# Kernel tuning notes

Measured on AMD Instinct MI355X. Metric: run time of the kernel, lower is better.

The kernel has to match this reference:

```python
import jax, jax.numpy as jnp
import numpy as np

D_MODEL = 1024
N_HEADS = 16
D_HEAD = D_MODEL // N_HEADS
LSR_RANK = 32
B, T = 2, 2048


def setup_inputs() -> dict:
    key = jax.random.key(0)
    ks = jax.random.split(key, 12)
    s = 1.0 / np.sqrt(D_MODEL)
    return {
        "x": jax.random.normal(ks[0], (B, T, D_MODEL), dtype=jnp.float32),
        "Wq": jax.random.normal(ks[1], (D_MODEL, D_MODEL), dtype=jnp.float32) * s,
        "bq": jnp.zeros((D_MODEL,), dtype=jnp.float32),
        "Wk": jax.random.normal(ks[2], (D_MODEL, D_MODEL), dtype=jnp.float32) * s,
        "bk": jnp.zeros((D_MODEL,), dtype=jnp.float32),
        "Wv": jax.random.normal(ks[3], (D_MODEL, D_MODEL), dtype=jnp.float32) * s,
        "bv": jnp.zeros((D_MODEL,), dtype=jnp.float32),
        "Wo": jax.random.normal(ks[4], (D_MODEL, D_MODEL), dtype=jnp.float32) * s,
        "bo": jnp.zeros((D_MODEL,), dtype=jnp.float32),
        "Wq_lsr": jax.random.normal(ks[5], (N_HEADS, D_HEAD, LSR_RANK), dtype=jnp.float32),
        "Wk_lsr": jax.random.normal(ks[6], (N_HEADS, D_HEAD, LSR_RANK), dtype=jnp.float32),
    }


def reference(x, Wq, bq, Wk, bk, Wv, bv, Wo, bo, Wq_lsr, Wk_lsr):
    Bn, Tn, dm = x.shape
    H, Dh, R = Wq_lsr.shape
    # q/k/v projections, split into heads: (B, H, T, Dh)
    def split_heads(y):
        return y.reshape(Bn, Tn, H, Dh).transpose(0, 2, 1, 3)
    q = split_heads(x @ Wq + bq)
    k = split_heads(x @ Wk + bk)
    v = split_heads(x @ Wv + bv)
    # low-rank projected scores: (Q Wq_lsr)(K Wk_lsr)^T / sqrt(R)
    q_lr = jnp.einsum('bhtd,hdr->bhtr', q, Wq_lsr)
    k_lr = jnp.einsum('bhtd,hdr->bhtr', k, Wk_lsr)
    scale = 1.0 / jnp.sqrt(jnp.float32(R))
    scores = jnp.einsum('bhir,bhjr->bhij', q_lr, k_lr) * scale
    # causal mask
    causal = jnp.tril(jnp.ones((Tn, Tn), dtype=bool))
    scores = jnp.where(causal[None, None], scores, -jnp.inf)
    attn = jax.nn.softmax(scores, axis=-1)
    out = jnp.einsum('bhij,bhjd->bhid', attn, v)  # (B, H, T, Dh)
    out = out.transpose(0, 2, 1, 3).reshape(Bn, Tn, dm)
    return out @ Wo + bo
```

## Files before the change

kernel.cpp:

```cpp
#include <hip/hip_runtime.h>
#include <math.h>

#define D_MODEL 1024
#define N_HEADS 16
#define D_HEAD  64
#define LSR_RANK 32
#define BATCH 2
#define SEQ 2048
#define M_TOT (BATCH*SEQ)

typedef __attribute__((ext_vector_type(8))) short short8v;
typedef __attribute__((ext_vector_type(4))) short short4v;
typedef __attribute__((ext_vector_type(4))) float f32x4;

static __device__ __forceinline__ ushort bfhi(float f) {
    union { float f; unsigned u; } c; c.f = f;
    return (ushort)(c.u >> 16);
}
static __device__ __forceinline__ float bff(ushort h) {
    union { unsigned u; float f; } c; c.u = ((unsigned)h) << 16;
    return c.f;
}
static __device__ __forceinline__ ushort f2bf_rn(float f) {
    union { float f; unsigned u; } c; c.f = f;
    unsigned r = c.u + 0x7FFF + ((c.u >> 16) & 1);
    return (ushort)(r >> 16);
}
static __device__ __forceinline__ void split8(const float4 a, const float4 b,
                                              short8v& h, short8v& l) {
    ushort h0 = bfhi(a.x), h1 = bfhi(a.y), h2 = bfhi(a.z), h3 = bfhi(a.w);
    ushort h4 = bfhi(b.x), h5 = bfhi(b.y), h6 = bfhi(b.z), h7 = bfhi(b.w);
    h[0] = (short)h0; h[1] = (short)h1; h[2] = (short)h2; h[3] = (short)h3;
    h[4] = (short)h4; h[5] = (short)h5; h[6] = (short)h6; h[7] = (short)h7;
    l[0] = (short)bfhi(a.x - bff(h0)); l[1] = (short)bfhi(a.y - bff(h1));
    l[2] = (short)bfhi(a.z - bff(h2)); l[3] = (short)bfhi(a.w - bff(h3));
    l[4] = (short)bfhi(b.x - bff(h4)); l[5] = (short)bfhi(b.y - bff(h5));
    l[6] = (short)bfhi(b.z - bff(h6)); l[7] = (short)bfhi(b.w - bff(h7));
}
static __device__ __forceinline__ void trunc8(const float4 a, const float4 b,
                                              short8v& h) {
    h[0] = (short)bfhi(a.x); h[1] = (short)bfhi(a.y);
    h[2] = (short)bfhi(a.z); h[3] = (short)bfhi(a.w);
    h[4] = (short)bfhi(b.x); h[5] = (short)bfhi(b.y);
    h[6] = (short)bfhi(b.z); h[7] = (short)bfhi(b.w);
}

__global__ __launch_bounds__(256) void eff_weight2(
    const float* __restrict__ Wq, const float* __restrict__ Wq_lsr,
    const float* __restrict__ Wk, const float* __restrict__ Wk_lsr,
    float* __restrict__ Weff_tmp)
{
    const int z = blockIdx.y;
    const float* W    = z ? Wk : Wq;
    const float* Wlsr = z ? Wk_lsr : Wq_lsr;
    const int base = z << 9;
    int idx = blockIdx.x * 256 + threadIdx.x;
    int k = idx >> 9;
    int c = idx & 511;
    int h = c >> 5;
    int r = c & 31;
    const float* wrow = W + (size_t)k * D_MODEL + h * D_HEAD;
    const float* lsr  = Wlsr + (size_t)h * D_HEAD * LSR_RANK + r;
    float acc = 0.f;
    #pragma unroll
    for (int d = 0; d < D_HEAD; ++d)
        acc = fmaf(wrow[d], lsr[d * LSR_RANK], acc);
    Weff_tmp[(size_t)k * 1024 + base + c] = acc;
}

__global__ __launch_bounds__(256) void eff_bias_kernel(
    const float* __restrict__ bq, const float* __restrict__ Wq_lsr,
    const float* __restrict__ bk, const float* __restrict__ Wk_lsr,
    const float* __restrict__ bv, float* __restrict__ bcat)
{
    int c = blockIdx.x * 256 + threadIdx.x;
    if (c < 1024) {
        const float* bias = (c < 512) ? bq : bk;
        const float* lsr  = (c < 512) ? Wq_lsr : Wk_lsr;
        int cc = c & 511;
        int h = cc >> 5, r = cc & 31;
        float acc = 0.f;
        #pragma unroll
        for (int d = 0; d < D_HEAD; ++d)
            acc = fmaf(bias[h * D_HEAD + d],
                       lsr[(size_t)h * D_HEAD * LSR_RANK + d * LSR_RANK + r], acc);
        bcat[c] = acc;
    } else {
        bcat[c] = bv[c - 1024];
    }
}

__global__ __launch_bounds__(256) void transpose2(
    const float* __restrict__ in0, float* __restrict__ out0,
    const float* __restrict__ in1, float* __restrict__ out1)
{
    const float* in  = blockIdx.z ? in1 : in0;
    float* out       = blockIdx.z ? out1 : out0;
    __shared__ float t[64][65];
    const int tid = threadIdx.x;
    const int r0 = blockIdx.y * 64, c0 = blockIdx.x * 64;
    const int tr = tid >> 4, tc = tid & 15;
    #pragma unroll
    for (int i = 0; i < 4; ++i) {
        float4 v = *(const float4*)&in[(size_t)(r0 + tr + i * 16) * 1024 + c0 + tc * 4];
        t[tr + i * 16][tc * 4 + 0] = v.x;
        t[tr + i * 16][tc * 4 + 1] = v.y;
        t[tr + i * 16][tc * 4 + 2] = v.z;
        t[tr + i * 16][tc * 4 + 3] = v.w;
    }
    __syncthreads();
    #pragma unroll
    for (int i = 0; i < 4; ++i) {
        float4 v;
        v.x = t[tc * 4 + 0][tr + i * 16];
        v.y = t[tc * 4 + 1][tr + i * 16];
        v.z = t[tc * 4 + 2][tr + i * 16];
        v.w = t[tc * 4 + 3][tr + i * 16];
        *(float4*)&out[(size_t)(c0 + tr + i * 16) * 1024 + r0 + tc * 4] = v;
    }
}

__global__ __launch_bounds__(256) void tsplit_rn1024(
    const float* __restrict__ in, ushort* __restrict__ out)
{
    __shared__ float t[64][65];
    const int tid = threadIdx.x;
    const int r0 = blockIdx.y * 64, c0 = blockIdx.x * 64;
    const int tr = tid >> 4, tc = tid & 15;
    #pragma unroll
    for (int i = 0; i < 4; ++i) {
        float4 v = *(const float4*)&in[(size_t)(r0 + tr + i * 16) * 1024 + c0 + tc * 4];
        t[tr + i * 16][tc * 4 + 0] = v.x;
        t[tr + i * 16][tc * 4 + 1] = v.y;
        t[tr + i * 16][tc * 4 + 2] = v.z;
        t[tr + i * 16][tc * 4 + 3] = v.w;
    }
    __syncthreads();
    #pragma unroll
    for (int i = 0; i < 4; ++i) {
        short4v hv = {(short)f2bf_rn(t[tc * 4 + 0][tr + i * 16]),
                      (short)f2bf_rn(t[tc * 4 + 1][tr + i * 16]),
                      (short)f2bf_rn(t[tc * 4 + 2][tr + i * 16]),
                      (short)f2bf_rn(t[tc * 4 + 3][tr + i * 16])};
        *(short4v*)&out[(size_t)(c0 + tr + i * 16) * 1024 + r0 + tc * 4] = hv;
    }
}

__global__ __launch_bounds__(256) void gemm_proj_fused(
    const float* __restrict__ x,
    const float* __restrict__ Wcat_t,
    const float* __restrict__ bcat,
    float* __restrict__ Yqk,
    short* __restrict__ Kth, short* __restrict__ Ktl,
    short* __restrict__ Vbf)
{
    __shared__ __align__(16) short Ah[128 * 40], Al[128 * 40];
    __shared__ __align__(16) short Bh[128 * 40], Bl[128 * 40];

    const int tid = threadIdx.x;
    const int bx = blockIdx.x;
    const int m0 = blockIdx.y * 128, n0 = bx * 128;
    const bool vhalf = (bx >= 8);
    const int wid = tid >> 6, wr = wid >> 1, wc = wid & 1;
    const int lane = tid & 63, fr = lane & 15, fq = lane >> 4;
    const int srow = tid >> 1;
    const int skq  = (tid & 1) << 4;

    f32x4 acc[4][4];
    #pragma unroll
    for (int i = 0; i < 4; ++i)
        #pragma unroll
        for (int j = 0; j < 4; ++j)
            acc[i][j] = (f32x4){0.f, 0.f, 0.f, 0.f};

    const float* Ag = x + (size_t)(m0 + srow) * 1024 + skq;
    const float* Bg = Wcat_t + (size_t)(n0 + srow) * 1024 + skq;
    short* pAh = &Ah[srow * 40 + skq];
    short* pAl = &Al[srow * 40 + skq];
    short* pBh = &Bh[srow * 40 + skq];
    short* pBl = &Bl[srow * 40 + skq];

    for (int k0 = 0; k0 < 1024; k0 += 32) {
        float4 a0 = *(const float4*)(Ag + k0);
        float4 a1 = *(const float4*)(Ag + k0 + 4);
        float4 a2 = *(const float4*)(Ag + k0 + 8);
        float4 a3 = *(const float4*)(Ag + k0 + 12);
        float4 b0 = *(const float4*)(Bg + k0);
        float4 b1 = *(const float4*)(Bg + k0 + 4);
        float4 b2 = *(const float4*)(Bg + k0 + 8);
        float4 b3 = *(const float4*)(Bg + k0 + 12);
        if (vhalf) {
            short8v h;
            trunc8(a0, a1, h); *(short8v*)pAh = h;
            trunc8(a2, a3, h); *(short8v*)(pAh + 8) = h;
            trunc8(b0, b1, h); *(short8v*)pBh = h;
            trunc8(b2, b3, h); *(short8v*)(pBh + 8) = h;
        } else {
            short8v h, l;
            split8(a0, a1, h, l);
            *(short8v*)pAh = h;  *(short8v*)pAl = l;
            split8(a2, a3, h, l);
            *(short8v*)(pAh + 8) = h;  *(short8v*)(pAl + 8) = l;
            split8(b0, b1, h, l);
            *(short8v*)pBh = h;  *(short8v*)pBl = l;
            split8(b2, b3, h, l);
            *(short8v*)(pBh + 8) = h;  *(short8v*)(pBl + 8) = l;
        }
        __syncthreads();

        short8v afh[4], bfh[4];
        #pragma unroll
        for (int fi = 0; fi < 4; ++fi)
            afh[fi] = *(const short8v*)&Ah[(wr * 64 + fi * 16 + fr) * 40 + fq * 8];
        #pragma unroll
        for (int bj = 0; bj < 4; ++bj)
            bfh[bj] = *(const short8v*)&Bh[(wc * 64 + bj * 16 + fr) * 40 + fq * 8];

        if (vhalf) {
            #pragma unroll
            for (int fi = 0; fi < 4; ++fi)
                #pragma unroll
                for (int bj = 0; bj < 4; ++bj)
                    acc[fi][bj] = __builtin_amdgcn_mfma_f32_16x16x32_bf16(
                        afh[fi], bfh[bj], acc[fi][bj], 0, 0, 0);
        } else {
            short8v afl[4], bfl[4];
            #pragma unroll
            for (int fi = 0; fi < 4; ++fi)
                afl[fi] = *(const short8v*)&Al[(wr * 64 + fi * 16 + fr) * 40 + fq * 8];
            #pragma unroll
            for (int bj = 0; bj < 4; ++bj)
                bfl[bj] = *(const short8v*)&Bl[(wc * 64 + bj * 16 + fr) * 40 + fq * 8];
            #pragma unroll
            for (int fi = 0; fi < 4; ++fi) {
                #pragma unroll
                for (int bj = 0; bj < 4; ++bj) {
                    acc[fi][bj] = __builtin_amdgcn_mfma_f32_16x16x32_bf16(
                        afh[fi], bfh[bj], acc[fi][bj], 0, 0, 0);
                    acc[fi][bj] = __builtin_amdgcn_mfma_f32_16x16x32_bf16(
                        afh[fi], bfl[bj], acc[fi][bj], 0, 0, 0);
                    acc[fi][bj] = __builtin_amdgcn_mfma_f32_16x16x32_bf16(
                        afl[fi], bfh[bj], acc[fi][bj], 0, 0, 0);
                }
            }
        }
        __syncthreads();
    }

    const int b = m0 >> 11;
    #pragma unroll
    for (int fi = 0; fi < 4; ++fi) {
        #pragma unroll
        for (int bj = 0; bj < 4; ++bj) {
            const int r = m0 + wr * 64 + fi * 16 + fq * 4;
            const int gcol = n0 + wc * 64 + bj * 16 + fr;
            const float bv_ = bcat[gcol];
            if (bx < 4) {
                #pragma unroll
                for (int j = 0; j < 4; ++j)
                    Yqk[(size_t)(r + j) * 1024 + gcol] = acc[fi][bj][j] + bv_;
            } else if (bx < 8) {
                const int kc = gcol - 512;
                const int h = kc >> 5, rr = kc & 31;
                short* oh = Kth + (((size_t)(b * 16 + h) * 2048) + (r & 2047)) * 32 + rr;
                short* ol = Ktl + (((size_t)(b * 16 + h) * 2048) + (r & 2047)) * 32 + rr;
                #pragma unroll
                for (int j = 0; j < 4; ++j) {
                    const float v = acc[fi][bj][j] + bv_;
                    const ushort vh = bfhi(v);
                    oh[j * 32] = (short)vh;
                    ol[j * 32] = (short)bfhi(v - bff(vh));
                }
            } else {
                const int vc = gcol - 1024;
                const int h = vc >> 6, d = vc & 63;
                short4v o = {(short)f2bf_rn(acc[fi][bj][0] + bv_),
                             (short)f2bf_rn(acc[fi][bj][1] + bv_),
                             (short)f2bf_rn(acc[fi][bj][2] + bv_),
                             (short)f2bf_rn(acc[fi][bj][3] + bv_)};
                *(short4v*)&Vbf[((size_t)(b * 16 + h) * 64 + d) * 2048 + (r & 2047)] = o;
            }
        }
    }
}

__global__ __launch_bounds__(256) void gemm_out_bf(
    const ushort* __restrict__ Obf,
    const ushort* __restrict__ Wot,
    const float* __restrict__ bo,
    float* __restrict__ out)
{
    __shared__ __align__(16) short Ah[128 * 40];
    __shared__ __align__(16) short Bh[128 * 40];

    const int tid = threadIdx.x;
    const int m0 = blockIdx.y * 128, n0 = blockIdx.x * 128;
    const int wid = tid >> 6, wr = wid >> 1, wc = wid & 1;
    const int lane = tid & 63, fr = lane & 15, fq = lane >> 4;
    const int srow = tid >> 1;
    const int skq  = (tid & 1) << 4;

    f32x4 acc[4][4];
    #pragma unroll
    for (int i = 0; i < 4; ++i)
        #pragma unroll
        for (int j = 0; j < 4; ++j)
            acc[i][j] = (f32x4){0.f, 0.f, 0.f, 0.f};

    const ushort* AgH = Obf + (size_t)(m0 + srow) * 1024 + skq;
    const ushort* BgH = Wot + (size_t)(n0 + srow) * 1024 + skq;
    short* pAh = &Ah[srow * 40 + skq];
    short* pBh = &Bh[srow * 40 + skq];

    for (int k0 = 0; k0 < 1024; k0 += 32) {
        *(short8v*)pAh       = *(const short8v*)(AgH + k0);
        *(short8v*)(pAh + 8) = *(const short8v*)(AgH + k0 + 8);
        *(short8v*)pBh       = *(const short8v*)(BgH + k0);
        *(short8v*)(pBh + 8) = *(const short8v*)(BgH + k0 + 8);
        __syncthreads();

        short8v afh[4], bfh[4];
        #pragma unroll
        for (int fi = 0; fi < 4; ++fi)
            afh[fi] = *(const short8v*)&Ah[(wr * 64 + fi * 16 + fr) * 40 + fq * 8];
        #pragma unroll
        for (int bj = 0; bj < 4; ++bj)
            bfh[bj] = *(const short8v*)&Bh[(wc * 64 + bj * 16 + fr) * 40 + fq * 8];
        #pragma unroll
        for (int fi = 0; fi < 4; ++fi)
            #pragma unroll
            for (int bj = 0; bj < 4; ++bj)
                acc[fi][bj] = __builtin_amdgcn_mfma_f32_16x16x32_bf16(
                    afh[fi], bfh[bj], acc[fi][bj], 0, 0, 0);
        __syncthreads();
    }

    #pragma unroll
    for (int fi = 0; fi < 4; ++fi) {
        #pragma unroll
        for (int bj = 0; bj < 4; ++bj) {
            const int r = m0 + wr * 64 + fi * 16 + fq * 4;
            const int c = n0 + wc * 64 + bj * 16 + fr;
            const float bv_ = bo[c];
            #pragma unroll
            for (int j = 0; j < 4; ++j)
                out[(size_t)(r + j) * 1024 + c] = acc[fi][bj][j] + bv_;
        }
    }
}

#define P_LD  68
#define MASKVAL (-1e30f)

__global__ __launch_bounds__(512) void flash_mfma(
    const float* __restrict__ Yqk,
    const short* __restrict__ Kth, const short* __restrict__ Ktl,
    const short* __restrict__ Vbf,
    ushort* __restrict__ Obf)
{
    const float scale = 0.1767766952966369f;
    const int L = blockIdx.x;
    const int bh = L & 31;
    const int qt = 31 - (L >> 5);
    const int b = bh >> 4, h = bh & 15;
    const int tid = threadIdx.x;
    const int w = tid >> 6;
    const int g = w & 3;
    const int p = w >> 2;
    const int lane = tid & 63;
    const int fr = lane & 15, fq = lane >> 4;

    __shared__ __align__(16) short Pall[8][16 * P_LD];
    __shared__ __align__(16) char exraw[4 * 64 * 80];
    short* Pw = &Pall[w][0];

    short8v aqh, aql;
    {
        const float* qp = Yqk + (size_t)(b * SEQ + qt * 64 + g * 16 + fr) * 1024
                          + h * 32 + fq * 8;
        split8(*(const float4*)qp, *(const float4*)(qp + 4), aqh, aql);
    }

    f32x4 acc0 = {0,0,0,0}, acc1 = {0,0,0,0}, acc2 = {0,0,0,0}, acc3 = {0,0,0,0};
    float m_[4], l_[4];
    #pragma unroll
    for (int r = 0; r < 4; ++r) { m_[r] = MASKVAL; l_[r] = 0.f; }

    const short* kb_h = Kth + (size_t)bh * 2048 * 32;
    const short* kb_l = Ktl + (size_t)bh * 2048 * 32;
    const short* vb   = Vbf + (size_t)bh * 64 * 2048;
    const int kidx = fr * 32 + fq * 8;
    const int vrow = fr * 2048 + fq * 8;

    for (int jt = p; jt <= qt; jt += 2) {
        const short* kp_h = kb_h + (size_t)jt * 64 * 32;
        const short* kp_l = kb_l + (size_t)jt * 64 * 32;
        short8v kh0 = *(const short8v*)&kp_h[kidx];
        short8v kh1 = *(const short8v*)&kp_h[kidx + 512];
        short8v kh2 = *(const short8v*)&kp_h[kidx + 1024];
        short8v kh3 = *(const short8v*)&kp_h[kidx + 1536];
        short8v kl0 = *(const short8v*)&kp_l[kidx];
        short8v kl1 = *(const short8v*)&kp_l[kidx + 512];
        short8v kl2 = *(const short8v*)&kp_l[kidx + 1024];
        short8v kl3 = *(const short8v*)&kp_l[kidx + 1536];
        const short* vp = vb + vrow + jt * 64;
        short8v v00 = *(const short8v*)&vp[0];
        short8v v01 = *(const short8v*)&vp[32];
        short8v v10 = *(const short8v*)&vp[16 * 2048];
        short8v v11 = *(const short8v*)&vp[16 * 2048 + 32];
        short8v v20 = *(const short8v*)&vp[32 * 2048];
        short8v v21 = *(const short8v*)&vp[32 * 2048 + 32];
        short8v v30 = *(const short8v*)&vp[48 * 2048];
        short8v v31 = *(const short8v*)&vp[48 * 2048 + 32];

        f32x4 s0 = {0,0,0,0}, s1 = {0,0,0,0}, s2 = {0,0,0,0}, s3 = {0,0,0,0};
        s0 = __builtin_amdgcn_mfma_f32_16x16x32_bf16(aqh, kh0, s0, 0, 0, 0);
        s0 = __builtin_amdgcn_mfma_f32_16x16x32_bf16(aqh, kl0, s0, 0, 0, 0);
        s0 = __builtin_amdgcn_mfma_f32_16x16x32_bf16(aql, kh0, s0, 0, 0, 0);
        s1 = __builtin_amdgcn_mfma_f32_16x16x32_bf16(aqh, kh1, s1, 0, 0, 0);
        s1 = __builtin_amdgcn_mfma_f32_16x16x32_bf16(aqh, kl1, s1, 0, 0, 0);
        s1 = __builtin_amdgcn_mfma_f32_16x16x32_bf16(aql, kh1, s1, 0, 0, 0);
        s2 = __builtin_amdgcn_mfma_f32_16x16x32_bf16(aqh, kh2, s2, 0, 0, 0);
        s2 = __builtin_amdgcn_mfma_f32_16x16x32_bf16(aqh, kl2, s2, 0, 0, 0);
        s2 = __builtin_amdgcn_mfma_f32_16x16x32_bf16(aql, kh2, s2, 0, 0, 0);
        s3 = __builtin_amdgcn_mfma_f32_16x16x32_bf16(aqh, kh3, s3, 0, 0, 0);
        s3 = __builtin_amdgcn_mfma_f32_16x16x32_bf16(aqh, kl3, s3, 0, 0, 0);
        s3 = __builtin_amdgcn_mfma_f32_16x16x32_bf16(aql, kh3, s3, 0, 0, 0);

        s0 *= scale; s1 *= scale; s2 *= scale; s3 *= scale;

        if (jt == qt) {
            #pragma unroll
            for (int r = 0; r < 4; ++r) {
                const int q_l = g * 16 + fq * 4 + r;
                s0[r] = (fr      <= q_l) ? s0[r] : MASKVAL;
                s1[r] = (16 + fr <= q_l) ? s1[r] : MASKVAL;
                s2[r] = (32 + fr <= q_l) ? s2[r] : MASKVAL;
                s3[r] = (48 + fr <= q_l) ? s3[r] : MASKVAL;
            }
        }

        float al[4];
        #pragma unroll
        for (int r = 0; r < 4; ++r) {
            float mt = fmaxf(fmaxf(s0[r], s1[r]), fmaxf(s2[r], s3[r]));
            mt = fmaxf(mt, __shfl_xor(mt, 1));
            mt = fmaxf(mt, __shfl_xor(mt, 2));
            mt = fmaxf(mt, __shfl_xor(mt, 4));
            mt = fmaxf(mt, __shfl_xor(mt, 8));
            const float mnew = fmaxf(m_[r], mt);
            al[r] = __expf(m_[r] - mnew);
            m_[r] = mnew;
            s0[r] = __expf(s0[r] - mnew);
            s1[r] = __expf(s1[r] - mnew);
            s2[r] = __expf(s2[r] - mnew);
            s3[r] = __expf(s3[r] - mnew);
            float ps = s0[r] + s1[r] + s2[r] + s3[r];
            ps += __shfl_xor(ps, 1);
            ps += __shfl_xor(ps, 2);
            ps += __shfl_xor(ps, 4);
            ps += __shfl_xor(ps, 8);
            l_[r] = l_[r] * al[r] + ps;
        }

        #pragma unroll
        for (int r = 0; r < 4; ++r) {
            const int prow = fq * 4 + r;
            Pw[prow * P_LD +      fr] = (short)f2bf_rn(s0[r]);
            Pw[prow * P_LD + 16 + fr] = (short)f2bf_rn(s1[r]);
            Pw[prow * P_LD + 32 + fr] = (short)f2bf_rn(s2[r]);
            Pw[prow * P_LD + 48 + fr] = (short)f2bf_rn(s3[r]);
        }
        #pragma unroll
        for (int r = 0; r < 4; ++r) {
            acc0[r] *= al[r]; acc1[r] *= al[r];
            acc2[r] *= al[r]; acc3[r] *= al[r];
        }
        short8v pa0 = *(const short8v*)&Pw[fr * P_LD + fq * 8];
        short8v pa1 = *(const short8v*)&Pw[fr * P_LD + 32 + fq * 8];

        acc0 = __builtin_amdgcn_mfma_f32_16x16x32_bf16(pa0, v00, acc0, 0, 0, 0);
        acc0 = __builtin_amdgcn_mfma_f32_16x16x32_bf16(pa1, v01, acc0, 0, 0, 0);
        acc1 = __builtin_amdgcn_mfma_f32_16x16x32_bf16(pa0, v10, acc1, 0, 0, 0);
        acc1 = __builtin_amdgcn_mfma_f32_16x16x32_bf16(pa1, v11, acc1, 0, 0, 0);
        acc2 = __builtin_amdgcn_mfma_f32_16x16x32_bf16(pa0, v20, acc2, 0, 0, 0);
        acc2 = __builtin_amdgcn_mfma_f32_16x16x32_bf16(pa1, v21, acc2, 0, 0, 0);
        acc3 = __builtin_amdgcn_mfma_f32_16x16x32_bf16(pa0, v30, acc3, 0, 0, 0);
        acc3 = __builtin_amdgcn_mfma_f32_16x16x32_bf16(pa1, v31, acc3, 0, 0, 0);
    }

    char* e = exraw + (size_t)(((g << 6) + lane) * 80);
    if (p == 1) {
        short8v a01, a23;
        a01[0] = (short)f2bf_rn(acc0[0]); a01[1] = (short)f2bf_rn(acc0[1]);
        a01[2] = (short)f2bf_rn(acc0[2]); a01[3] = (short)f2bf_rn(acc0[3]);
        a01[4] = (short)f2bf_rn(acc1[0]); a01[5] = (short)f2bf_rn(acc1[1]);
        a01[6] = (short)f2bf_rn(acc1[2]); a01[7] = (short)f2bf_rn(acc1[3]);
        a23[0] = (short)f2bf_rn(acc2[0]); a23[1] = (short)f2bf_rn(acc2[1]);
        a23[2] = (short)f2bf_rn(acc2[2]); a23[3] = (short)f2bf_rn(acc2[3]);
        a23[4] = (short)f2bf_rn(acc3[0]); a23[5] = (short)f2bf_rn(acc3[1]);
        a23[6] = (short)f2bf_rn(acc3[2]); a23[7] = (short)f2bf_rn(acc3[3]);
        *(short8v*)(e)      = a01;
        *(short8v*)(e + 16) = a23;
        *(f32x4*)(e + 32) = (f32x4){m_[0], m_[1], m_[2], m_[3]};
        *(f32x4*)(e + 48) = (f32x4){l_[0], l_[1], l_[2], l_[3]};
    }
    __syncthreads();
    if (p == 0) {
        short8v a01 = *(const short8v*)(e);
        short8v a23 = *(const short8v*)(e + 16);
        f32x4 m1 = *(const f32x4*)(e + 32);
        f32x4 l1 = *(const f32x4*)(e + 48);
        #pragma unroll
        for (int r = 0; r < 4; ++r) {
            const float mm = fmaxf(m_[r], m1[r]);
            const float a0 = __expf(m_[r] - mm);
            const float a1 = __expf(m1[r] - mm);
            const float inv = 1.f / (l_[r] * a0 + l1[r] * a1);
            const float b0 = bff((ushort)a01[r]);
            const float b1 = bff((ushort)a01[4 + r]);
            const float b2 = bff((ushort)a23[r]);
            const float b3 = bff((ushort)a23[4 + r]);
            const int trow = qt * 64 + g * 16 + fq * 4 + r;
            ushort* op = Obf + (size_t)(b * SEQ + trow) * 1024 + h * 64;
            op[     fr] = f2bf_rn((acc0[r] * a0 + b0 * a1) * inv);
            op[16 + fr] = f2bf_rn((acc1[r] * a0 + b1 * a1) * inv);
            op[32 + fr] = f2bf_rn((acc2[r] * a0 + b2 * a1) * inv);
            op[48 + fr] = f2bf_rn((acc3[r] * a0 + b3 * a1) * inv);
        }
    }
}

extern "C" void kernel_launch(void* const* d_in, const int* in_sizes, int n_in,
                              void* d_out, int out_size, void* d_ws, size_t ws_size,
                              hipStream_t stream)
{
    const float* x      = (const float*)d_in[0];
    const float* Wq     = (const float*)d_in[1];
    const float* bq     = (const float*)d_in[2];
    const float* Wk     = (const float*)d_in[3];
    const float* bk     = (const float*)d_in[4];
    const float* Wv     = (const float*)d_in[5];
    const float* bv     = (const float*)d_in[6];
    const float* Wo     = (const float*)d_in[7];
    const float* bo     = (const float*)d_in[8];
    const float* Wq_lsr = (const float*)d_in[9];
    const float* Wk_lsr = (const float*)d_in[10];
    float* out = (float*)d_out;

    float* ws     = (float*)d_ws;
    float* Wcat_t = ws;
    float* bcat   = Wcat_t + (size_t)2048 * 1024;
    float* Yqk    = bcat + 2048;
    float* Weff_tmp = Yqk;
    short* Kth    = (short*)(Yqk + (size_t)M_TOT * 1024);
    short* Ktl    = Kth + (size_t)32 * 2048 * 32;
    short* Vbf    = Ktl + (size_t)32 * 2048 * 32;
    ushort* Obf   = (ushort*)(Vbf + (size_t)32 * 64 * 2048);
    ushort* Wot   = (ushort*)Wcat_t;

    eff_weight2<<<dim3(2048, 2), 256, 0, stream>>>(Wq, Wq_lsr, Wk, Wk_lsr, Weff_tmp);
    eff_bias_kernel<<<8, 256, 0, stream>>>(bq, Wq_lsr, bk, Wk_lsr, bv, bcat);

    transpose2<<<dim3(16, 16, 2), 256, 0, stream>>>(
        Weff_tmp, Wcat_t, Wv, Wcat_t + (size_t)1024 * 1024);

    gemm_proj_fused<<<dim3(16, 32), 256, 0, stream>>>(
        x, Wcat_t, bcat, Yqk, Kth, Ktl, Vbf);

    tsplit_rn1024<<<dim3(16, 16), 256, 0, stream>>>(Wo, Wot);

    flash_mfma<<<1024, 512, 0, stream>>>(Yqk, Kth, Ktl, Vbf, Obf);

    gemm_out_bf<<<dim3(8, 32), 256, 0, stream>>>(Obf, Wot, bo, out);
}
```

Baseline: 215.7 us.

## Process two query tiles per flash-attention block to reuse K/V loads

Each flash attention block now handles two adjacent 64-row query tiles, so every K and V tile loaded from global memory feeds both tiles' score and PV MFMAs. The grid is halved to 512 blocks. This cuts global K/V traffic roughly in half but doubles the accumulator registers per thread, which may lower occupancy. It also leaves fewer blocks to spread across the GPU's compute units.

```diff
diff --git a/kernel.cpp b/kernel.cpp
--- a/kernel.cpp
+++ b/kernel.cpp
@@ -361,7 +361,8 @@
     const float scale = 0.1767766952966369f;
     const int L = blockIdx.x;
     const int bh = L & 31;
-    const int qt = 31 - (L >> 5);
+    const int qp = 15 - (L >> 5);
+    const int qtA = 2 * qp, qtB = 2 * qp + 1;
     const int b = bh >> 4, h = bh & 15;
     const int tid = threadIdx.x;
     const int w = tid >> 6;
@@ -374,17 +375,24 @@
     __shared__ __align__(16) char exraw[4 * 64 * 80];
     short* Pw = &Pall[w][0];
 
-    short8v aqh, aql;
+    short8v aqhA, aqlA, aqhB, aqlB;
     {
-        const float* qp = Yqk + (size_t)(b * SEQ + qt * 64 + g * 16 + fr) * 1024
-                          + h * 32 + fq * 8;
-        split8(*(const float4*)qp, *(const float4*)(qp + 4), aqh, aql);
-    }
-
-    f32x4 acc0 = {0,0,0,0}, acc1 = {0,0,0,0}, acc2 = {0,0,0,0}, acc3 = {0,0,0,0};
-    float m_[4], l_[4];
-    #pragma unroll
-    for (int r = 0; r < 4; ++r) { m_[r] = MASKVAL; l_[r] = 0.f; }
+        const float* qpA = Yqk + (size_t)(b * SEQ + qtA * 64 + g * 16 + fr) * 1024
+                           + h * 32 + fq * 8;
+        split8(*(const float4*)qpA, *(const float4*)(qpA + 4), aqhA, aqlA);
+        const float* qpB = Yqk + (size_t)(b * SEQ + qtB * 64 + g * 16 + fr) * 1024
+                           + h * 32 + fq * 8;
+        split8(*(const float4*)qpB, *(const float4*)(qpB + 4), aqhB, aqlB);
+    }
+
+    f32x4 accA0 = {0,0,0,0}, accA1 = {0,0,0,0}, accA2 = {0,0,0,0}, accA3 = {0,0,0,0};
+    f32x4 accB0 = {0,0,0,0}, accB1 = {0,0,0,0}, accB2 = {0,0,0,0}, accB3 = {0,0,0,0};
+    float mA[4], lA[4], mB[4], lB[4];
+    #pragma unroll
+    for (int r = 0; r < 4; ++r) {
+        mA[r] = MASKVAL; lA[r] = 0.f;
+        mB[r] = MASKVAL; lB[r] = 0.f;
+    }
 
     const short* kb_h = Kth + (size_t)bh * 2048 * 32;
     const short* kb_l = Ktl + (size_t)bh * 2048 * 32;
@@ -392,7 +400,7 @@
     const int kidx = fr * 32 + fq * 8;
     const int vrow = fr * 2048 + fq * 8;
 
-    for (int jt = p; jt <= qt; jt += 2) {
+    for (int jt = p; jt <= qtB; jt += 2) {
         const short* kp_h = kb_h + (size_t)jt * 64 * 32;
         const short* kp_l = kb_l + (size_t)jt * 64 * 32;
         short8v kh0 = *(const short8v*)&kp_h[kidx];
@@ -413,97 +421,177 @@
         short8v v30 = *(const short8v*)&vp[48 * 2048];
         short8v v31 = *(const short8v*)&vp[48 * 2048 + 32];
 
-        f32x4 s0 = {0,0,0,0}, s1 = {0,0,0,0}, s2 = {0,0,0,0}, s3 = {0,0,0,0};
-        s0 = __builtin_amdgcn_mfma_f32_16x16x32_bf16(aqh, kh0, s0, 0, 0, 0);
-        s0 = __builtin_amdgcn_mfma_f32_16x16x32_bf16(aqh, kl0, s0, 0, 0, 0);
-        s0 = __builtin_amdgcn_mfma_f32_16x16x32_bf16(aql, kh0, s0, 0, 0, 0);
-        s1 = __builtin_amdgcn_mfma_f32_16x16x32_bf16(aqh, kh1, s1, 0, 0, 0);
-        s1 = __builtin_amdgcn_mfma_f32_16x16x32_bf16(aqh, kl1, s1, 0, 0, 0);
-        s1 = __builtin_amdgcn_mfma_f32_16x16x32_bf16(aql, kh1, s1, 0, 0, 0);
-        s2 = __builtin_amdgcn_mfma_f32_16x16x32_bf16(aqh, kh2, s2, 0, 0, 0);
-        s2 = __builtin_amdgcn_mfma_f32_16x16x32_bf16(aqh, kl2, s2, 0, 0, 0);
-        s2 = __builtin_amdgcn_mfma_f32_16x16x32_bf16(aql, kh2, s2, 0, 0, 0);
-        s3 = __builtin_amdgcn_mfma_f32_16x16x32_bf16(aqh, kh3, s3, 0, 0, 0);
-        s3 = __builtin_amdgcn_mfma_f32_16x16x32_bf16(aqh, kl3, s3, 0, 0, 0);
-        s3 = __builtin_amdgcn_mfma_f32_16x16x32_bf16(aql, kh3, s3, 0, 0, 0);
-
-        s0 *= scale; s1 *= scale; s2 *= scale; s3 *= scale;
-
-        if (jt == qt) {
+        if (jt <= qtA) {
+            f32x4 s0 = {0,0,0,0}, s1 = {0,0,0,0}, s2 = {0,0,0,0}, s3 = {0,0,0,0};
+            s0 = __builtin_amdgcn_mfma_f32_16x16x32_bf16(aqhA, kh0, s0, 0, 0, 0);
+            s0 = __builtin_amdgcn_mfma_f32_16x16x32_bf16(aqhA, kl0, s0, 0, 0, 0);
+            s0 = __builtin_amdgcn_mfma_f32_16x16x32_bf16(aqlA, kh0, s0, 0, 0, 0);
+            s1 = __builtin_amdgcn_mfma_f32_16x16x32_bf16(aqhA, kh1, s1, 0, 0, 0);
+            s1 = __builtin_amdgcn_mfma_f32_16x16x32_bf16(aqhA, kl1, s1, 0, 0, 0);
+            s1 = __builtin_amdgcn_mfma_f32_16x16x32_bf16(aqlA, kh1, s1, 0, 0, 0);
+            s2 = __builtin_amdgcn_mfma_f32_16x16x32_bf16(aqhA, kh2, s2, 0, 0, 0);
+            s2 = __builtin_amdgcn_mfma_f32_16x16x32_bf16(aqhA, kl2, s2, 0, 0, 0);
+            s2 = __builtin_amdgcn_mfma_f32_16x16x32_bf16(aqlA, kh2, s2, 0, 0, 0);
+            s3 = __builtin_amdgcn_mfma_f32_16x16x32_bf16(aqhA, kh3, s3, 0, 0, 0);
+            s3 = __builtin_amdgcn_mfma_f32_16x16x32_bf16(aqhA, kl3, s3, 0, 0, 0);
+            s3 = __builtin_amdgcn_mfma_f32_16x16x32_bf16(aqlA, kh3, s3, 0, 0, 0);
+
+            s0 *= scale; s1 *= scale; s2 *= scale; s3 *= scale;
+
+            if (jt == qtA) {
+                #pragma unroll
+                for (int r = 0; r < 4; ++r) {
+                    const int q_l = g * 16 + fq * 4 + r;
+                    s0[r] = (fr      <= q_l) ? s0[r] : MASKVAL;
+                    s1[r] = (16 + fr <= q_l) ? s1[r] : MASKVAL;
+                    s2[r] = (32 + fr <= q_l) ? s2[r] : MASKVAL;
+                    s3[r] = (48 + fr <= q_l) ? s3[r] : MASKVAL;
+                }
+            }
+
+            float al[4];
             #pragma unroll
             for (int r = 0; r < 4; ++r) {
-                const int q_l = g * 16 + fq * 4 + r;
-                s0[r] = (fr      <= q_l) ? s0[r] : MASKVAL;
-                s1[r] = (16 + fr <= q_l) ? s1[r] : MASKVAL;
-                s2[r] = (32 + fr <= q_l) ? s2[r] : MASKVAL;
-                s3[r] = (48 + fr <= q_l) ? s3[r] : MASKVAL;
-            }
+                float mt = fmaxf(fmaxf(s0[r], s1[r]), fmaxf(s2[r], s3[r]));
+                mt = fmaxf(mt, __shfl_xor(mt, 1));
+                mt = fmaxf(mt, __shfl_xor(mt, 2));
+                mt = fmaxf(mt, __shfl_xor(mt, 4));
+                mt = fmaxf(mt, __shfl_xor(mt, 8));
+                const float mnew = fmaxf(mA[r], mt);
+                al[r] = __expf(mA[r] - mnew);
+                mA[r] = mnew;
+                s0[r] = __expf(s0[r] - mnew);
+                s1[r] = __expf(s1[r] - mnew);
+                s2[r] = __expf(s2[r] - mnew);
+                s3[r] = __expf(s3[r] - mnew);
+                float ps = s0[r] + s1[r] + s2[r] + s3[r];
+                ps += __shfl_xor(ps, 1);
+                ps += __shfl_xor(ps, 2);
+                ps += __shfl_xor(ps, 4);
+                ps += __shfl_xor(ps, 8);
+                lA[r] = lA[r] * al[r] + ps;
+            }
+
+            #pragma unroll
+            for (int r = 0; r < 4; ++r) {
+                const int prow = fq * 4 + r;
+                Pw[prow * P_LD +      fr] = (short)f2bf_rn(s0[r]);
+                Pw[prow * P_LD + 16 + fr] = (short)f2bf_rn(s1[r]);
+                Pw[prow * P_LD + 32 + fr] = (short)f2bf_rn(s2[r]);
+                Pw[prow * P_LD + 48 + fr] = (short)f2bf_rn(s3[r]);
+            }
+            #pragma unroll
+            for (int r = 0; r < 4; ++r) {
+                accA0[r] *= al[r]; accA1[r] *= al[r];
+                accA2[r] *= al[r]; accA3[r] *= al[r];
+            }
+            short8v pa0 = *(const short8v*)&Pw[fr * P_LD + fq * 8];
+            short8v pa1 = *(const short8v*)&Pw[fr * P_LD + 32 + fq * 8];
+
+            accA0 = __builtin_amdgcn_mfma_f32_16x16x32_bf16(pa0, v00, accA0, 0, 0, 0);
+            accA0 = __builtin_amdgcn_mfma_f32_16x16x32_bf16(pa1, v01, accA0, 0, 0, 0);
+            accA1 = __builtin_amdgcn_mfma_f32_16x16x32_bf16(pa0, v10, accA1, 0, 0, 0);
+            accA1 = __builtin_amdgcn_mfma_f32_16x16x32_bf16(pa1, v11, accA1, 0, 0, 0);
+            accA2 = __builtin_amdgcn_mfma_f32_16x16x32_bf16(pa0, v20, accA2, 0, 0, 0);
+            accA2 = __builtin_amdgcn_mfma_f32_16x16x32_bf16(pa1, v21, accA2, 0, 0, 0);
+            accA3 = __builtin_amdgcn_mfma_f32_16x16x32_bf16(pa0, v30, accA3, 0, 0, 0);
+            accA3 = __builtin_amdgcn_mfma_f32_16x16x32_bf16(pa1, v31, accA3, 0, 0, 0);
         }
 
-        float al[4];
-        #pragma unroll
-        for (int r = 0; r < 4; ++r) {
-            float mt = fmaxf(fmaxf(s0[r], s1[r]), fmaxf(s2[r], s3[r]));
-            mt = fmaxf(mt, __shfl_xor(mt, 1));
-            mt = fmaxf(mt, __shfl_xor(mt, 2));
-            mt = fmaxf(mt, __shfl_xor(mt, 4));
-            mt = fmaxf(mt, __shfl_xor(mt, 8));
-            const float mnew = fmaxf(m_[r], mt);
-            al[r] = __expf(m_[r] - mnew);
-            m_[r] = mnew;
-            s0[r] = __expf(s0[r] - mnew);
-            s1[r] = __expf(s1[r] - mnew);
-            s2[r] = __expf(s2[r] - mnew);
-            s3[r] = __expf(s3[r] - mnew);
-            float ps = s0[r] + s1[r] + s2[r] + s3[r];
-            ps += __shfl_xor(ps, 1);
-            ps += __shfl_xor(ps, 2);
-            ps += __shfl_xor(ps, 4);
-            ps += __shfl_xor(ps, 8);
-            l_[r] = l_[r] * al[r] + ps;
+        {
+            f32x4 s0 = {0,0,0,0}, s1 = {0,0,0,0}, s2 = {0,0,0,0}, s3 = {0,0,0,0};
+            s0 = __builtin_amdgcn_mfma_f32_16x16x32_bf16(aqhB, kh0, s0, 0, 0, 0);
+            s0 = __builtin_amdgcn_mfma_f32_16x16x32_bf16(aqhB, kl0, s0, 0, 0, 0);
+            s0 = __builtin_amdgcn_mfma_f32_16x16x32_bf16(aqlB, kh0, s0, 0, 0, 0);
+            s1 = __builtin_amdgcn_mfma_f32_16x16x32_bf16(aqhB, kh1, s1, 0, 0, 0);
+            s1 = __builtin_amdgcn_mfma_f32_16x16x32_bf16(aqhB, kl1, s1, 0, 0, 0);
+            s1 = __builtin_amdgcn_mfma_f32_16x16x32_bf16(aqlB, kh1, s1, 0, 0, 0);
+            s2 = __builtin_amdgcn_mfma_f32_16x16x32_bf16(aqhB, kh2, s2, 0, 0, 0);
+            s2 = __builtin_amdgcn_mfma_f32_16x16x32_bf16(aqhB, kl2, s2, 0, 0, 0);
+            s2 = __builtin_amdgcn_mfma_f32_16x16x32_bf16(aqlB, kh2, s2, 0, 0, 0);
+            s3 = __builtin_amdgcn_mfma_f32_16x16x32_bf16(aqhB, kh3, s3, 0, 0, 0);
+            s3 = __builtin_amdgcn_mfma_f32_16x16x32_bf16(aqhB, kl3, s3, 0, 0, 0);
+            s3 = __builtin_amdgcn_mfma_f32_16x16x32_bf16(aqlB, kh3, s3, 0, 0, 0);
+
+            s0 *= scale; s1 *= scale; s2 *= scale; s3 *= scale;
+
+            if (jt == qtB) {
+                #pragma unroll
+                for (int r = 0; r < 4; ++r) {
+                    const int q_l = g * 16 + fq * 4 + r;
+                    s0[r] = (fr      <= q_l) ? s0[r] : MASKVAL;
+                    s1[r] = (16 + fr <= q_l) ? s1[r] : MASKVAL;
+                    s2[r] = (32 + fr <= q_l) ? s2[r] : MASKVAL;
+                    s3[r] = (48 + fr <= q_l) ? s3[r] : MASKVAL;
+                }
+            }
+
+            float al[4];
+            #pragma unroll
+            for (int r = 0; r < 4; ++r) {
+                float mt = fmaxf(fmaxf(s0[r], s1[r]), fmaxf(s2[r], s3[r]));
+                mt = fmaxf(mt, __shfl_xor(mt, 1));
+                mt = fmaxf(mt, __shfl_xor(mt, 2));
+                mt = fmaxf(mt, __shfl_xor(mt, 4));
+                mt = fmaxf(mt, __shfl_xor(mt, 8));
+                const float mnew = fmaxf(mB[r], mt);
+                al[r] = __expf(mB[r] - mnew);
+                mB[r] = mnew;
+                s0[r] = __expf(s0[r] - mnew);
+                s1[r] = __expf(s1[r] - mnew);
+                s2[r] = __expf(s2[r] - mnew);
+                s3[r] = __expf(s3[r] - mnew);
+                float ps = s0[r] + s1[r] + s2[r] + s3[r];
+                ps += __shfl_xor(ps, 1);
+                ps += __shfl_xor(ps, 2);
+                ps += __shfl_xor(ps, 4);
+                ps += __shfl_xor(ps, 8);
+                lB[r] = lB[r] * al[r] + ps;
+            }
+
+            #pragma unroll
+            for (int r = 0; r < 4; ++r) {
+                const int prow = fq * 4 + r;
+                Pw[prow * P_LD +      fr] = (short)f2bf_rn(s0[r]);
+                Pw[prow * P_LD + 16 + fr] = (short)f2bf_rn(s1[r]);
+                Pw[prow * P_LD + 32 + fr] = (short)f2bf_rn(s2[r]);
+                Pw[prow * P_LD + 48 + fr] = (short)f2bf_rn(s3[r]);
+            }
+            #pragma unroll
+            for (int r = 0; r < 4; ++r) {
+                accB0[r] *= al[r]; accB1[r] *= al[r];
+                accB2[r] *= al[r]; accB3[r] *= al[r];
+            }
+            short8v pa0 = *(const short8v*)&Pw[fr * P_LD + fq * 8];
+            short8v pa1 = *(const short8v*)&Pw[fr * P_LD + 32 + fq * 8];
+
+            accB0 = __builtin_amdgcn_mfma_f32_16x16x32_bf16(pa0, v00, accB0, 0, 0, 0);
+            accB0 = __builtin_amdgcn_mfma_f32_16x16x32_bf16(pa1, v01, accB0, 0, 0, 0);
+            accB1 = __builtin_amdgcn_mfma_f32_16x16x32_bf16(pa0, v10, accB1, 0, 0, 0);
+            accB1 = __builtin_amdgcn_mfma_f32_16x16x32_bf16(pa1, v11, accB1, 0, 0, 0);
+            accB2 = __builtin_amdgcn_mfma_f32_16x16x32_bf16(pa0, v20, accB2, 0, 0, 0);
+            accB2 = __builtin_amdgcn_mfma_f32_16x16x32_bf16(pa1, v21, accB2, 0, 0, 0);
+            accB3 = __builtin_amdgcn_mfma_f32_16x16x32_bf16(pa0, v30, accB3, 0, 0, 0);
+            accB3 = __builtin_amdgcn_mfma_f32_16x16x32_bf16(pa1, v31, accB3, 0, 0, 0);
         }
-
-        #pragma unroll
-        for (int r = 0; r < 4; ++r) {
-            const int prow = fq * 4 + r;
-            Pw[prow * P_LD +      fr] = (short)f2bf_rn(s0[r]);
-            Pw[prow * P_LD + 16 + fr] = (short)f2bf_rn(s1[r]);
-            Pw[prow * P_LD + 32 + fr] = (short)f2bf_rn(s2[r]);
-            Pw[prow * P_LD + 48 + fr] = (short)f2bf_rn(s3[r]);
-        }
-        #pragma unroll
-        for (int r = 0; r < 4; ++r) {
-            acc0[r] *= al[r]; acc1[r] *= al[r];
-            acc2[r] *= al[r]; acc3[r] *= al[r];
-        }
-        short8v pa0 = *(const short8v*)&Pw[fr * P_LD + fq * 8];
-        short8v pa1 = *(const short8v*)&Pw[fr * P_LD + 32 + fq * 8];
-
-        acc0 = __builtin_amdgcn_mfma_f32_16x16x32_bf16(pa0, v00, acc0, 0, 0, 0);
-        acc0 = __builtin_amdgcn_mfma_f32_16x16x32_bf16(pa1, v01, acc0, 0, 0, 0);
-        acc1 = __builtin_amdgcn_mfma_f32_16x16x32_bf16(pa0, v10, acc1, 0, 0, 0);
-        acc1 = __builtin_amdgcn_mfma_f32_16x16x32_bf16(pa1, v11, acc1, 0, 0, 0);
-        acc2 = __builtin_amdgcn_mfma_f32_16x16x32_bf16(pa0, v20, acc2, 0, 0, 0);
-        acc2 = __builtin_amdgcn_mfma_f32_16x16x32_bf16(pa1, v21, acc2, 0, 0, 0);
-        acc3 = __builtin_amdgcn_mfma_f32_16x16x32_bf16(pa0, v30, acc3, 0, 0, 0);
-        acc3 = __builtin_amdgcn_mfma_f32_16x16x32_bf16(pa1, v31, acc3, 0, 0, 0);
     }
 
     char* e = exraw + (size_t)(((g << 6) + lane) * 80);
+
     if (p == 1) {
         short8v a01, a23;
-        a01[0] = (short)f2bf_rn(acc0[0]); a01[1] = (short)f2bf_rn(acc0[1]);
-        a01[2] = (short)f2bf_rn(acc0[2]); a01[3] = (short)f2bf_rn(acc0[3]);
-        a01[4] = (short)f2bf_rn(acc1[0]); a01[5] = (short)f2bf_rn(acc1[1]);
-        a01[6] = (short)f2bf_rn(acc1[2]); a01[7] = (short)f2bf_rn(acc1[3]);
-        a23[0] = (short)f2bf_rn(acc2[0]); a23[1] = (short)f2bf_rn(acc2[1]);
-        a23[2] = (short)f2bf_rn(acc2[2]); a23[3] = (short)f2bf_rn(acc2[3]);
-        a23[4] = (short)f2bf_rn(acc3[0]); a23[5] = (short)f2bf_rn(acc3[1]);
-        a23[6] = (short)f2bf_rn(acc3[2]); a23[7] = (short)f2bf_rn(acc3[3]);
+        a01[0] = (short)f2bf_rn(accA0[0]); a01[1] = (short)f2bf_rn(accA0[1]);
+        a01[2] = (short)f2bf_rn(accA0[2]); a01[3] = (short)f2bf_rn(accA0[3]);
+        a01[4] = (short)f2bf_rn(accA1[0]); a01[5] = (short)f2bf_rn(accA1[1]);
+        a01[6] = (short)f2bf_rn(accA1[2]); a01[7] = (short)f2bf_rn(accA1[3]);
+        a23[0] = (short)f2bf_rn(accA2[0]); a23[1] = (short)f2bf_rn(accA2[1]);
+        a23[2] = (short)f2bf_rn(accA2[2]); a23[3] = (short)f2bf_rn(accA2[3]);
+        a23[4] = (short)f2bf_rn(accA3[0]); a23[5] = (short)f2bf_rn(accA3[1]);
+        a23[6] = (short)f2bf_rn(accA3[2]); a23[7] = (short)f2bf_rn(accA3[3]);
         *(short8v*)(e)      = a01;
         *(short8v*)(e + 16) = a23;
-        *(f32x4*)(e + 32) = (f32x4){m_[0], m_[1], m_[2], m_[3]};
-        *(f32x4*)(e + 48) = (f32x4){l_[0], l_[1], l_[2], l_[3]};
+        *(f32x4*)(e + 32) = (f32x4){mA[0], mA[1], mA[2], mA[3]};
+        *(f32x4*)(e + 48) = (f32x4){lA[0], lA[1], lA[2], lA[3]};
     }
     __syncthreads();
     if (p == 0) {
@@ -513,20 +601,61 @@
         f32x4 l1 = *(const f32x4*)(e + 48);
         #pragma unroll
         for (int r = 0; r < 4; ++r) {
-            const float mm = fmaxf(m_[r], m1[r]);
-            const float a0 = __expf(m_[r] - mm);
+            const float mm = fmaxf(mA[r], m1[r]);
+            const float a0 = __expf(mA[r] - mm);
             const float a1 = __expf(m1[r] - mm);
-            const float inv = 1.f / (l_[r] * a0 + l1[r] * a1);
+            const float inv = 1.f / (lA[r] * a0 + l1[r] * a1);
             const float b0 = bff((ushort)a01[r]);
             const float b1 = bff((ushort)a01[4 + r]);
             const float b2 = bff((ushort)a23[r]);
             const float b3 = bff((ushort)a23[4 + r]);
-            const int trow = qt * 64 + g * 16 + fq * 4 + r;
+            const int trow = qtA * 64 + g * 16 + fq * 4 + r;
             ushort* op = Obf + (size_t)(b * SEQ + trow) * 1024 + h * 64;
-            op[     fr] = f2bf_rn((acc0[r] * a0 + b0 * a1) * inv);
-            op[16 + fr] = f2bf_rn((acc1[r] * a0 + b1 * a1) * inv);
-            op[32 + fr] = f2bf_rn((acc2[r] * a0 + b2 * a1) * inv);
-            op[48 + fr] = f2bf_rn((acc3[r] * a0 + b3 * a1) * inv);
+            op[     fr] = f2bf_rn((accA0[r] * a0 + b0 * a1) * inv);
+            op[16 + fr] = f2bf_rn((accA1[r] * a0 + b1 * a1) * inv);
+            op[32 + fr] = f2bf_rn((accA2[r] * a0 + b2 * a1) * inv);
+            op[48 + fr] = f2bf_rn((accA3[r] * a0 + b3 * a1) * inv);
+        }
+    }
+    __syncthreads();
+
+    if (p == 1) {
+        short8v a01, a23;
+        a01[0] = (short)f2bf_rn(accB0[0]); a01[1] = (short)f2bf_rn(accB0[1]);
+        a01[2] = (short)f2bf_rn(accB0[2]); a01[3] = (short)f2bf_rn(accB0[3]);
+        a01[4] = (short)f2bf_rn(accB1[0]); a01[5] = (short)f2bf_rn(accB1[1]);
+        a01[6] = (short)f2bf_rn(accB1[2]); a01[7] = (short)f2bf_rn(accB1[3]);
+        a23[0] = (short)f2bf_rn(accB2[0]); a23[1] = (short)f2bf_rn(accB2[1]);
+        a23[2] = (short)f2bf_rn(accB2[2]); a23[3] = (short)f2bf_rn(accB2[3]);
+        a23[4] = (short)f2bf_rn(accB3[0]); a23[5] = (short)f2bf_rn(accB3[1]);
+        a23[6] = (short)f2bf_rn(accB3[2]); a23[7] = (short)f2bf_rn(accB3[3]);
+        *(short8v*)(e)      = a01;
+        *(short8v*)(e + 16) = a23;
+        *(f32x4*)(e + 32) = (f32x4){mB[0], mB[1], mB[2], mB[3]};
+        *(f32x4*)(e + 48) = (f32x4){lB[0], lB[1], lB[2], lB[3]};
+    }
+    __syncthreads();
+    if (p == 0) {
+        short8v a01 = *(const short8v*)(e);
+        short8v a23 = *(const short8v*)(e + 16);
+        f32x4 m1 = *(const f32x4*)(e + 32);
+        f32x4 l1 = *(const f32x4*)(e + 48);
+        #pragma unroll
+        for (int r = 0; r < 4; ++r) {
+            const float mm = fmaxf(mB[r], m1[r]);
+            const float a0 = __expf(mB[r] - mm);
+            const float a1 = __expf(m1[r] - mm);
+            const float inv = 1.f / (lB[r] * a0 + l1[r] * a1);
+            const float b0 = bff((ushort)a01[r]);
+            const float b1 = bff((ushort)a01[4 + r]);
+            const float b2 = bff((ushort)a23[r]);
+            const float b3 = bff((ushort)a23[4 + r]);
+            const int trow = qtB * 64 + g * 16 + fq * 4 + r;
+            ushort* op = Obf + (size_t)(b * SEQ + trow) * 1024 + h * 64;
+            op[     fr] = f2bf_rn((accB0[r] * a0 + b0 * a1) * inv);
+            op[16 + fr] = f2bf_rn((accB1[r] * a0 + b1 * a1) * inv);
+            op[32 + fr] = f2bf_rn((accB2[r] * a0 + b2 * a1) * inv);
+            op[48 + fr] = f2bf_rn((accB3[r] * a0 + b3 * a1) * inv);
         }
     }
 }
@@ -570,7 +699,7 @@
 
     tsplit_rn1024<<<dim3(16, 16), 256, 0, stream>>>(Wo, Wot);
 
-    flash_mfma<<<1024, 512, 0, stream>>>(Yqk, Kth, Ktl, Vbf, Obf);
+    flash_mfma<<<512, 512, 0, stream>>>(Yqk, Kth, Ktl, Vbf, Obf);
 
     gemm_out_bf<<<dim3(8, 32), 256, 0, stream>>>(Obf, Wot, bo, out);
 }
```

Result: faster. 186.8 us (-13.4%).
